# Kernel optimization log

Measured on AMD Instinct MI355X. Metric: run time of the kernel, lower is better.

The kernel has to match this reference:

```python
import jax, jax.numpy as jnp
import numpy as np
from jax import lax

B, N, C, HEADS = 4096, 49, 256, 8
HD = C // HEADS
SCALE = HD ** -0.5
BRANCHES = [(1, 0), (2, 0), (3, 1), (4, 2)]  # (dilation, padding) for d1..d4


def setup_inputs() -> dict:
    key = jax.random.key(0)
    ks = jax.random.split(key, 24)
    f = lambda i, shape: jax.random.normal(ks[i], shape, dtype=jnp.float32) * 0.05
    inp = {"x": jax.random.normal(ks[0], (B, N, C), dtype=jnp.float32)}
    inp["wq"] = f(1, (C, C)); inp["bq"] = f(2, (C,))
    for j in range(4):
        inp[f"wd{j+1}"] = f(3 + 4 * j, (C, 1, 3, 3))
        inp[f"bd{j+1}"] = f(4 + 4 * j, (C,))
        inp[f"wp{j+1}"] = f(5 + 4 * j, (2 * C, C))
        inp[f"bp{j+1}"] = f(6 + 4 * j, (2 * C,))
    inp["wproj"] = f(19, (C, C)); inp["bproj"] = f(20, (C,))
    return inp


def _branch(x4, wd, bd, wp, bp, dil, pad):
    # depthwise 3x3 stride-2 dilated conv
    d = lax.conv_general_dilated(
        x4, wd, window_strides=(2, 2), padding=[(pad, pad), (pad, pad)],
        rhs_dilation=(dil, dil), dimension_numbers=('NCHW', 'OIHW', 'NCHW'),
        feature_group_count=C) + bd[None, :, None, None]
    # pointwise 1x1 conv C -> 2C
    p = jnp.einsum('oc,bchw->bohw', wp, d) + bp[None, :, None, None]
    # replicate torch's reshape(B,C,-1).permute(0,2,1).reshape(B,-1,2,h,hd).permute(2,0,3,1,4)
    p = p.reshape(B, C, -1).transpose(0, 2, 1)
    p = p.reshape(B, -1, 2, HEADS, HD).transpose(2, 0, 3, 1, 4)
    return p[0], p[1]  # k, v: (B, HEADS, hw, HD)


def _forward(x, wq, bq, wd1, bd1, wp1, bp1, wd2, bd2, wp2, bp2,
             wd3, bd3, wp3, bp3, wd4, bd4, wp4, bp4, wproj, bproj):
    H = int(N ** 0.5)
    x4 = x.transpose(0, 2, 1).reshape(B, C, H, H)
    params = [(wd1, bd1, wp1, bp1), (wd2, bd2, wp2, bp2),
              (wd3, bd3, wp3, bp3), (wd4, bd4, wp4, bp4)]
    ks_, vs_ = [], []
    for (wd, bd, wp, bp), (dil, pad) in zip(params, BRANCHES):
        k_, v_ = _branch(x4, wd, bd, wp, bp, dil, pad)
        ks_.append(k_); vs_.append(v_)
    k = jnp.concatenate(ks_, axis=2)  # (B, HEADS, 21, HD)
    v = jnp.concatenate(vs_, axis=2)
    q = (jnp.einsum('bnc,oc->bno', x, wq) + bq)
    q = q.reshape(B, N, HEADS, HD).transpose(0, 2, 1, 3) * SCALE  # (B, H, N, HD)
    attn = jax.nn.softmax(jnp.einsum('bhnd,bhmd->bhnm', q, k), axis=-1)
    out = jnp.einsum('bhnm,bhmd->bhnd', attn, v)
    out = out.transpose(0, 2, 1, 3).reshape(B, N, C)
    return jnp.einsum('bnc,oc->bno', out, wproj) + bproj


def reference(x, wq, bq, wd1, bd1, wp1, bp1, wd2, bd2, wp2, bp2,
              wd3, bd3, wp3, bp3, wd4, bd4, wp4, bp4, wproj, bproj):
    return _forward(x, wq, bq, wd1, bd1, wp1, bp1, wd2, bd2, wp2, bp2,
                    wd3, bd3, wp3, bp3, wd4, bd4, wp4, bp4, wproj, bproj)
```

## Files before the change

### kernel.cpp

```cpp
#include <hip/hip_runtime.h>
#include <stdint.h>

typedef __attribute__((ext_vector_type(8))) short bf16x8;
typedef __attribute__((ext_vector_type(8))) unsigned short u16x8;
typedef __attribute__((ext_vector_type(4))) float f32x4;
typedef __attribute__((ext_vector_type(2))) uint32_t u32x2;

#define DEV __device__ __forceinline__

constexpr size_t WQ_PK    = 0;
constexpr size_t WPROJ_PK = 65536;
constexpr size_t WP_PK    = 131072;
constexpr size_t KVBUF    = 655360;

constexpr float SCALE_Q  = 0.17677669529663687f;

DEV uint16_t f2bf(float f){
  uint32_t u = __builtin_bit_cast(uint32_t, f);
  u += 0x7fffu + ((u >> 16) & 1u);
  return (uint16_t)(u >> 16);
}

DEV uint32_t cvtpk(float a, float b){
  uint32_t r;
  asm("v_cvt_pk_bf16_f32 %0, %1, %2" : "=v"(r) : "v"(a), "v"(b));
  return r;
}

DEV u16x8 extract_par(u16x8 a, u16x8 b, uint32_t sel){
  union U { u16x8 v; uint32_t d[4]; } A, B, R;
  A.v = a; B.v = b;
  R.d[0] = __builtin_amdgcn_perm(A.d[1], A.d[0], sel);
  R.d[1] = __builtin_amdgcn_perm(A.d[3], A.d[2], sel);
  R.d[2] = __builtin_amdgcn_perm(B.d[1], B.d[0], sel);
  R.d[3] = __builtin_amdgcn_perm(B.d[3], B.d[2], sel);
  return R.v;
}

__global__ __launch_bounds__(256) void k_prepack(
    const float* __restrict__ wq,  const float* __restrict__ wp1,
    const float* __restrict__ wp2, const float* __restrict__ wp3,
    const float* __restrict__ wp4, const float* __restrict__ wproj,
    uint16_t* __restrict__ ws)
{
  int f = blockIdx.x * 256 + threadIdx.x;
  const float* src; uint16_t* dst; int g;
  if (f < 8192)       { src = wq;    dst = ws + WQ_PK;    g = f; }
  else if (f < 16384) { src = wproj; dst = ws + WPROJ_PK; g = f - 8192; }
  else {
    int j = (f - 16384) >> 14;
    src = j == 0 ? wp1 : j == 1 ? wp2 : j == 2 ? wp3 : wp4;
    dst = ws + WP_PK + (size_t)j * 131072;
    g = (f - 16384) & 16383;
  }
  int l = g & 63, kt = (g >> 6) & 7, nt = g >> 9;
  int n  = nt * 16 + (l & 15);
  int k0 = kt * 32 + (l >> 4) * 8;
  const float* s = src + (size_t)n * 256 + k0;
  u16x8 v;
  #pragma unroll
  for (int j = 0; j < 8; ++j) v[j] = f2bf(s[j]);
  *reinterpret_cast<u16x8*>(dst + (size_t)g * 8) = v;
}

__global__ __launch_bounds__(512, 2) void k_kv(
    const float* __restrict__ x,
    const float* __restrict__ wd1, const float* __restrict__ bd1, const float* __restrict__ bp1,
    const float* __restrict__ wd2, const float* __restrict__ bd2, const float* __restrict__ bp2,
    const float* __restrict__ wd3, const float* __restrict__ bd3, const float* __restrict__ bp3,
    const float* __restrict__ wd4, const float* __restrict__ bd4, const float* __restrict__ bp4,
    const uint16_t* __restrict__ ws, uint16_t* __restrict__ kvbuf)
{
  extern __shared__ char smem[];
  const int t = threadIdx.x, lane = t & 63, w = t >> 6;
  const int q4 = lane >> 4, c15 = lane & 15;
  const int b0 = blockIdx.x * 8;

  constexpr int DILA[4] = {1,2,3,4}, PADA[4] = {0,0,1,2}, OWA[4] = {3,2,2,2};
  constexpr int HWA[4]  = {9,4,4,4}, OFFA[4] = {0,9,13,17}, MTA[4] = {5,2,2,2};

  {
    const int c = t & 255, half = t >> 8;
    for (int pass = 0; pass < 4; ++pass){
      const int bh = pass * 2 + half;
      float xr[49];
      #pragma unroll
      for (int p = 0; p < 49; ++p)
        xr[p] = x[((size_t)(b0 + bh) * 49 + p) * 256 + c];
      #pragma unroll
      for (int j = 0; j < 4; ++j){
        const float* wdp = j==0?wd1:j==1?wd2:j==2?wd3:wd4;
        const float* bdp = j==0?bd1:j==1?bd2:j==2?bd3:bd4;
        float wv[9];
        #pragma unroll
        for (int q = 0; q < 9; ++q) wv[q] = wdp[c * 9 + q];
        const float bdv = bdp[c];
        #pragma unroll
        for (int oy = 0; oy < OWA[j]; ++oy)
        #pragma unroll
        for (int ox = 0; ox < OWA[j]; ++ox){
          float acc = bdv;
          #pragma unroll
          for (int ky = 0; ky < 3; ++ky){
            const int yy = oy * 2 - PADA[j] + ky * DILA[j];
            if (yy < 0 || yy > 6) continue;
            #pragma unroll
            for (int kx = 0; kx < 3; ++kx){
              const int xx = ox * 2 - PADA[j] + kx * DILA[j];
              if (xx < 0 || xx > 6) continue;
              acc += xr[yy * 7 + xx] * wv[ky * 3 + kx];
            }
          }
          const int row = bh * 21 + OFFA[j] + oy * OWA[j] + ox;
          *reinterpret_cast<uint16_t*>(smem + ((row * 512 + c * 2) ^ ((row & 7) << 4))) = f2bf(acc);
        }
      }
    }
  }
  __syncthreads();

  #pragma unroll
  for (int j = 0; j < 4; ++j){
    const uint16_t* pk = ws + WP_PK + (size_t)j * 131072;
    const float* bpp = j==0?bp1:j==1?bp2:j==2?bp3:bp4;
    const int hw = HWA[j], off = OFFA[j], MV = hw * 8, ST = MTA[j];
    for (int st = 0; st < ST; ++st){
      const int sl = st * 16 + c15;
      const bool sv = sl < MV;
      const int svc = sv ? sl : 0;
      const int bh = svc / hw, sp = svc - bh * hw;
      const int arow = bh * 21 + off + sp;
      f32x4 acc[4] = {};
      #pragma unroll
      for (int kt = 0; kt < 8; ++kt){
        bf16x8 bfr = *reinterpret_cast<const bf16x8*>(smem + ((arow * 512 + kt * 64 + q4 * 16) ^ ((arow & 7) << 4)));
        #pragma unroll
        for (int ot = 0; ot < 4; ++ot){
          bf16x8 aw = *reinterpret_cast<const bf16x8*>(pk + (size_t)(((w * 4 + ot) * 8 + kt) * 64 + lane) * 8);
          acc[ot] = __builtin_amdgcn_mfma_f32_16x16x32_bf16(aw, bfr, acc[ot], 0, 0, 0);
        }
      }
      if (sv){
        const size_t grow = ((size_t)(b0 + bh) * 21 + off + sp) * 512;
        #pragma unroll
        for (int ot = 0; ot < 4; ++ot){
          const int ob = w * 64 + ot * 16 + q4 * 4;
          const f32x4 vb = *reinterpret_cast<const f32x4*>(bpp + ob);
          u32x2 pkv;
          pkv[0] = cvtpk(acc[ot][0] + vb[0], acc[ot][1] + vb[1]);
          pkv[1] = cvtpk(acc[ot][2] + vb[2], acc[ot][3] + vb[3]);
          *reinterpret_cast<u32x2*>(kvbuf + grow + ob) = pkv;
        }
      }
    }
  }
}

__global__ __launch_bounds__(512, 4) void k_attn(
    const float* __restrict__ x, const float* __restrict__ bq,
    const float* __restrict__ bproj, const uint16_t* __restrict__ ws,
    float* __restrict__ out)
{
  extern __shared__ char smem[];
  constexpr int OSB = 32768;
  const int t = threadIdx.x, lane = t & 63, w = t >> 6;
  const int q4 = lane >> 4, c15 = lane & 15;
  const size_t b = blockIdx.x;
  const uint16_t* wq_pk    = ws + WQ_PK;
  const uint16_t* wproj_pk = ws + WPROJ_PK;
  const uint16_t* kvbuf    = ws + KVBUF;

  const int sh4 = t >> 7, m = (t >> 2) & 31, dch = (t & 3) * 8;
  const bool mv = m < 21;
  uint32_t selK = 0x05040100u, selV = 0x05040100u;
  const uint16_t *rk = kvbuf, *rv = kvbuf;
  if (mv){
    int off, hw;
    if (m < 9)       { off = 0;  hw = 9; }
    else if (m < 13) { off = 9;  hw = 4; }
    else if (m < 17) { off = 13; hw = 4; }
    else             { off = 17; hw = 4; }
    const int ml = m - off;
    const int c2k = 2 * ml,     ek = c2k >= hw ? 1 : 0, sk = c2k - ek * hw;
    const int c2v = 2 * ml + 1, ev = c2v >= hw ? 1 : 0, sv = c2v - ev * hw;
    selK = ek ? 0x07060302u : 0x05040100u;
    selV = ev ? 0x07060302u : 0x05040100u;
    const int o0 = 2 * (sh4 * 32 + dch);
    rk = kvbuf + (b * 21 + off + sk) * 512 + o0;
    rv = kvbuf + (b * 21 + off + sv) * 512 + o0;
  }
  u16x8 L0 = {}, L1 = {}, L2 = {}, L3 = {};
  if (mv){
    L0 = *reinterpret_cast<const u16x8*>(rk);
    L1 = *reinterpret_cast<const u16x8*>(rk + 8);
    L2 = *reinterpret_cast<const u16x8*>(rv);
    L3 = *reinterpret_cast<const u16x8*>(rv + 8);
  }

  {
    const int r = t >> 3, c0 = (t & 7) * 32;
    u16x8 vv[4] = {};
    if (r < 49){
      const float* src = x + (b * 49 + r) * 256 + c0;
      #pragma unroll
      for (int jj = 0; jj < 4; ++jj){
        f32x4 f0 = *reinterpret_cast<const f32x4*>(src + jj * 8);
        f32x4 f1 = *reinterpret_cast<const f32x4*>(src + jj * 8 + 4);
        union { u16x8 v; uint32_t d[4]; } R;
        R.d[0] = cvtpk(f0[0], f0[1]);
        R.d[1] = cvtpk(f0[2], f0[3]);
        R.d[2] = cvtpk(f1[0], f1[1]);
        R.d[3] = cvtpk(f1[2], f1[3]);
        vv[jj] = R.v;
      }
    }
    #pragma unroll
    for (int jj = 0; jj < 4; ++jj)
      *reinterpret_cast<u16x8*>(smem + ((r * 512 + c0 * 2 + jj * 16) ^ ((r & 7) << 4))) = vv[jj];
  }
  __syncthreads();

  f32x4 qacc[2][4] = {};
  #pragma unroll 2
  for (int kt = 0; kt < 8; ++kt){
    bf16x8 bx[4];
    #pragma unroll
    for (int nt = 0; nt < 4; ++nt){
      const int row = nt * 16 + c15;
      bx[nt] = *reinterpret_cast<const bf16x8*>(smem + ((row * 512 + kt * 64 + q4 * 16) ^ ((row & 7) << 4)));
    }
    #pragma unroll
    for (int mt = 0; mt < 2; ++mt){
      bf16x8 aw = *reinterpret_cast<const bf16x8*>(wq_pk + (size_t)(((w * 2 + mt) * 8 + kt) * 64 + lane) * 8);
      #pragma unroll
      for (int nt = 0; nt < 4; ++nt)
        qacc[mt][nt] = __builtin_amdgcn_mfma_f32_16x16x32_bf16(aw, bx[nt], qacc[mt][nt], 0, 0, 0);
    }
  }
  #pragma unroll
  for (int mt = 0; mt < 2; ++mt){
    const int ob = w * 32 + mt * 16 + q4 * 4;
    const f32x4 vb = *reinterpret_cast<const f32x4*>(bq + ob);
    #pragma unroll
    for (int nt = 0; nt < 4; ++nt){
      const int row = nt * 16 + c15;
      u32x2 pkq;
      pkq[0] = cvtpk((qacc[mt][nt][0] + vb[0]) * SCALE_Q, (qacc[mt][nt][1] + vb[1]) * SCALE_Q);
      pkq[1] = cvtpk((qacc[mt][nt][2] + vb[2]) * SCALE_Q, (qacc[mt][nt][3] + vb[3]) * SCALE_Q);
      *reinterpret_cast<u32x2*>(smem + OSB + ((row * 512 + ob * 2) ^ ((row & 7) << 4))) = pkq;
    }
  }
  __syncthreads();

  for (int p = 0; p < 2; ++p){
    {
      u16x8 kf = extract_par(L0, L1, selK);
      u16x8 vf = extract_par(L2, L3, selV);
      *reinterpret_cast<u16x8*>(smem + sh4 * 2048 + ((m * 64 + dch * 2) ^ ((m & 7) << 4))) = kf;
      #pragma unroll
      for (int jj = 0; jj < 8; ++jj){
        const int d = dch + jj;
        *reinterpret_cast<uint16_t*>(smem + 8192 + sh4 * 2048 + ((d * 64 + m * 2) ^ ((d & 7) << 4))) = vf[jj];
      }
      if (p == 0 && mv){
        L0 = *reinterpret_cast<const u16x8*>(rk + 256);
        L1 = *reinterpret_cast<const u16x8*>(rk + 264);
        L2 = *reinterpret_cast<const u16x8*>(rv + 256);
        L3 = *reinterpret_cast<const u16x8*>(rv + 264);
      }
    }
    __syncthreads();

    const int h4 = w >> 1, wh = w & 1;
    const int hcol = (p * 4 + h4) * 64;
    const int pabase = 16384 + h4 * 4096;

    bf16x8 bk[2];
    #pragma unroll
    for (int nt = 0; nt < 2; ++nt){
      const int m0 = nt * 16 + c15;
      bk[nt] = *reinterpret_cast<const bf16x8*>(smem + h4 * 2048 + ((m0 * 64 + q4 * 16) ^ ((m0 & 7) << 4)));
    }
    f32x4 sacc[2][2];
    #pragma unroll
    for (int mt = 0; mt < 2; ++mt){
      const int row = wh * 32 + mt * 16 + c15;
      bf16x8 aq = *reinterpret_cast<const bf16x8*>(smem + OSB + ((row * 512 + hcol + q4 * 16) ^ ((row & 7) << 4)));
      #pragma unroll
      for (int nt = 0; nt < 2; ++nt){
        f32x4 z = {};
        sacc[mt][nt] = __builtin_amdgcn_mfma_f32_16x16x32_bf16(aq, bk[nt], z, 0, 0, 0);
      }
    }
    const bool ok1 = c15 < 5;
    #pragma unroll
    for (int mt = 0; mt < 2; ++mt)
      #pragma unroll
      for (int i = 0; i < 4; ++i){
        const float s0 = sacc[mt][0][i];
        const float s1 = sacc[mt][1][i];
        float mx = fmaxf(s0, ok1 ? s1 : -3.0e38f);
        #pragma unroll
        for (int dd = 1; dd < 16; dd <<= 1) mx = fmaxf(mx, __shfl_xor(mx, dd));
        const float e0 = __expf(s0 - mx);
        const float e1 = ok1 ? __expf(s1 - mx) : 0.f;
        float sm = e0 + e1;
        #pragma unroll
        for (int dd = 1; dd < 16; dd <<= 1) sm += __shfl_xor(sm, dd);
        const float inv = 1.0f / sm;
        const int pr = wh * 32 + mt * 16 + q4 * 4 + i;
        *reinterpret_cast<uint16_t*>(smem + pabase + ((pr * 64 + c15 * 2) ^ ((pr & 7) << 4))) = f2bf(e0 * inv);
        *reinterpret_cast<uint16_t*>(smem + pabase + ((pr * 64 + (c15 + 16) * 2) ^ ((pr & 7) << 4))) = f2bf(e1 * inv);
      }
    f32x4 oacc[2][2];
    #pragma unroll
    for (int mt = 0; mt < 2; ++mt){
      const int pr = wh * 32 + mt * 16 + c15;
      bf16x8 ap = *reinterpret_cast<const bf16x8*>(smem + pabase + ((pr * 64 + q4 * 16) ^ ((pr & 7) << 4)));
      #pragma unroll
      for (int nt = 0; nt < 2; ++nt){
        const int d0 = nt * 16 + c15;
        bf16x8 bv = *reinterpret_cast<const bf16x8*>(smem + 8192 + h4 * 2048 + ((d0 * 64 + q4 * 16) ^ ((d0 & 7) << 4)));
        f32x4 z = {};
        oacc[mt][nt] = __builtin_amdgcn_mfma_f32_16x16x32_bf16(ap, bv, z, 0, 0, 0);
      }
    }
    #pragma unroll
    for (int mt = 0; mt < 2; ++mt)
      #pragma unroll
      for (int nt = 0; nt < 2; ++nt)
        #pragma unroll
        for (int i = 0; i < 4; ++i){
          const int row = wh * 32 + mt * 16 + q4 * 4 + i;
          const int colb = hcol + (nt * 16 + c15) * 2;
          *reinterpret_cast<uint16_t*>(smem + OSB + ((row * 512 + colb) ^ ((row & 7) << 4))) = f2bf(oacc[mt][nt][i]);
        }
    __syncthreads();
  }

  f32x4 pacc[2][4] = {};
  #pragma unroll 2
  for (int kt = 0; kt < 8; ++kt){
    bf16x8 bo[4];
    #pragma unroll
    for (int nt = 0; nt < 4; ++nt){
      const int row = nt * 16 + c15;
      bo[nt] = *reinterpret_cast<const bf16x8*>(smem + OSB + ((row * 512 + kt * 64 + q4 * 16) ^ ((row & 7) << 4)));
    }
    #pragma unroll
    for (int mt = 0; mt < 2; ++mt){
      bf16x8 aw = *reinterpret_cast<const bf16x8*>(wproj_pk + (size_t)(((w * 2 + mt) * 8 + kt) * 64 + lane) * 8);
      #pragma unroll
      for (int nt = 0; nt < 4; ++nt)
        pacc[mt][nt] = __builtin_amdgcn_mfma_f32_16x16x32_bf16(aw, bo[nt], pacc[mt][nt], 0, 0, 0);
    }
  }
  #pragma unroll
  for (int mt = 0; mt < 2; ++mt){
    const int ob = w * 32 + mt * 16 + q4 * 4;
    const f32x4 vb = *reinterpret_cast<const f32x4*>(bproj + ob);
    #pragma unroll
    for (int nt = 0; nt < 4; ++nt){
      const int n = nt * 16 + c15;
      if (n < 49)
        *reinterpret_cast<f32x4*>(out + (b * 49 + n) * 256 + ob) = pacc[mt][nt] + vb;
    }
  }
}

extern "C" void kernel_launch(void* const* d_in, const int* in_sizes, int n_in,
                              void* d_out, int out_size, void* d_ws, size_t ws_size,
                              hipStream_t stream)
{
  const float* x     = (const float*)d_in[0];
  const float* wq    = (const float*)d_in[1];
  const float* bq    = (const float*)d_in[2];
  const float* wd1   = (const float*)d_in[3];
  const float* bd1   = (const float*)d_in[4];
  const float* wp1   = (const float*)d_in[5];
  const float* bp1   = (const float*)d_in[6];
  const float* wd2   = (const float*)d_in[7];
  const float* bd2   = (const float*)d_in[8];
  const float* wp2   = (const float*)d_in[9];
  const float* bp2   = (const float*)d_in[10];
  const float* wd3   = (const float*)d_in[11];
  const float* bd3   = (const float*)d_in[12];
  const float* wp3   = (const float*)d_in[13];
  const float* bp3   = (const float*)d_in[14];
  const float* wd4   = (const float*)d_in[15];
  const float* bd4   = (const float*)d_in[16];
  const float* wp4   = (const float*)d_in[17];
  const float* bp4   = (const float*)d_in[18];
  const float* wproj = (const float*)d_in[19];
  const float* bproj = (const float*)d_in[20];
  uint16_t* ws = (uint16_t*)d_ws;
  float* out = (float*)d_out;

  k_prepack<<<320, 256, 0, stream>>>(wq, wp1, wp2, wp3, wp4, wproj, ws);
  k_kv<<<512, 512, 86016, stream>>>(x, wd1, bd1, bp1, wd2, bd2, bp2,
                                    wd3, bd3, bp3, wd4, bd4, bp4,
                                    ws, ws + KVBUF);
  k_attn<<<4096, 512, 65536, stream>>>(x, bq, bproj, ws, out);
}
```

Baseline: 329.8 us.

## Shrink attention LDS footprint and process two heads per pass to raise occupancy

The attention kernel now reuses the x staging buffer for Q/output, with an extra barrier before the Q writes, which cuts dynamic LDS from 64KB to 48KB. The launch-bounds occupancy hint goes from 4 to 6 blocks. Heads are now processed two per pass over four passes instead of four per pass over two, and each thread loads only a K or a V fragment, which halves the prefetch registers. The aim is more resident blocks per CU, at the cost of extra barriers and passes that add serialization.

```diff
diff --git a/kernel.cpp b/kernel.cpp
--- a/kernel.cpp
+++ b/kernel.cpp
@@ -156,13 +156,12 @@
   }
 }
 
-__global__ __launch_bounds__(512, 4) void k_attn(
+__global__ __launch_bounds__(512, 6) void k_attn(
     const float* __restrict__ x, const float* __restrict__ bq,
     const float* __restrict__ bproj, const uint16_t* __restrict__ ws,
     float* __restrict__ out)
 {
   extern __shared__ char smem[];
-  constexpr int OSB = 32768;
   const int t = threadIdx.x, lane = t & 63, w = t >> 6;
   const int q4 = lane >> 4, c15 = lane & 15;
   const size_t b = blockIdx.x;
@@ -170,10 +169,11 @@
   const uint16_t* wproj_pk = ws + WPROJ_PK;
   const uint16_t* kvbuf    = ws + KVBUF;
 
-  const int sh4 = t >> 7, m = (t >> 2) & 31, dch = (t & 3) * 8;
+  const int dch = (t & 3) * 8, m = (t >> 2) & 31, unit = t >> 7;
+  const int hh_s = unit >> 1, kind = unit & 1;
   const bool mv = m < 21;
-  uint32_t selK = 0x05040100u, selV = 0x05040100u;
-  const uint16_t *rk = kvbuf, *rv = kvbuf;
+  uint32_t sel = 0x05040100u;
+  const uint16_t* rg = kvbuf;
   if (mv){
     int off, hw;
     if (m < 9)       { off = 0;  hw = 9; }
@@ -181,20 +181,15 @@
     else if (m < 17) { off = 13; hw = 4; }
     else             { off = 17; hw = 4; }
     const int ml = m - off;
-    const int c2k = 2 * ml,     ek = c2k >= hw ? 1 : 0, sk = c2k - ek * hw;
-    const int c2v = 2 * ml + 1, ev = c2v >= hw ? 1 : 0, sv = c2v - ev * hw;
-    selK = ek ? 0x07060302u : 0x05040100u;
-    selV = ev ? 0x07060302u : 0x05040100u;
-    const int o0 = 2 * (sh4 * 32 + dch);
-    rk = kvbuf + (b * 21 + off + sk) * 512 + o0;
-    rv = kvbuf + (b * 21 + off + sv) * 512 + o0;
-  }
-  u16x8 L0 = {}, L1 = {}, L2 = {}, L3 = {};
+    const int c2 = 2 * ml + kind;
+    const int e = c2 >= hw ? 1 : 0, s = c2 - e * hw;
+    sel = e ? 0x07060302u : 0x05040100u;
+    rg = kvbuf + (b * 21 + off + s) * 512 + 2 * (hh_s * 32 + dch);
+  }
+  u16x8 L0 = {}, L1 = {};
   if (mv){
-    L0 = *reinterpret_cast<const u16x8*>(rk);
-    L1 = *reinterpret_cast<const u16x8*>(rk + 8);
-    L2 = *reinterpret_cast<const u16x8*>(rv);
-    L3 = *reinterpret_cast<const u16x8*>(rv + 8);
+    L0 = *reinterpret_cast<const u16x8*>(rg);
+    L1 = *reinterpret_cast<const u16x8*>(rg + 8);
   }
 
   {
@@ -237,6 +232,8 @@
         qacc[mt][nt] = __builtin_amdgcn_mfma_f32_16x16x32_bf16(aw, bx[nt], qacc[mt][nt], 0, 0, 0);
     }
   }
+  __syncthreads();
+
   #pragma unroll
   for (int mt = 0; mt < 2; ++mt){
     const int ob = w * 32 + mt * 16 + q4 * 4;
@@ -247,94 +244,83 @@
       u32x2 pkq;
       pkq[0] = cvtpk((qacc[mt][nt][0] + vb[0]) * SCALE_Q, (qacc[mt][nt][1] + vb[1]) * SCALE_Q);
       pkq[1] = cvtpk((qacc[mt][nt][2] + vb[2]) * SCALE_Q, (qacc[mt][nt][3] + vb[3]) * SCALE_Q);
-      *reinterpret_cast<u32x2*>(smem + OSB + ((row * 512 + ob * 2) ^ ((row & 7) << 4))) = pkq;
+      *reinterpret_cast<u32x2*>(smem + ((row * 512 + ob * 2) ^ ((row & 7) << 4))) = pkq;
     }
   }
   __syncthreads();
 
-  for (int p = 0; p < 2; ++p){
+  const int hh = w >> 2, wh2 = w & 3;
+  for (int p = 0; p < 4; ++p){
     {
-      u16x8 kf = extract_par(L0, L1, selK);
-      u16x8 vf = extract_par(L2, L3, selV);
-      *reinterpret_cast<u16x8*>(smem + sh4 * 2048 + ((m * 64 + dch * 2) ^ ((m & 7) << 4))) = kf;
-      #pragma unroll
-      for (int jj = 0; jj < 8; ++jj){
-        const int d = dch + jj;
-        *reinterpret_cast<uint16_t*>(smem + 8192 + sh4 * 2048 + ((d * 64 + m * 2) ^ ((d & 7) << 4))) = vf[jj];
-      }
-      if (p == 0 && mv){
-        L0 = *reinterpret_cast<const u16x8*>(rk + 256);
-        L1 = *reinterpret_cast<const u16x8*>(rk + 264);
-        L2 = *reinterpret_cast<const u16x8*>(rv + 256);
-        L3 = *reinterpret_cast<const u16x8*>(rv + 264);
+      u16x8 vfr = {};
+      if (mv) vfr = extract_par(L0, L1, sel);
+      if (kind == 0){
+        *reinterpret_cast<u16x8*>(smem + 32768 + hh_s * 2048 + ((m * 64 + dch * 2) ^ ((m & 7) << 4))) = vfr;
+      } else {
+        #pragma unroll
+        for (int jj = 0; jj < 8; ++jj){
+          const int d = dch + jj;
+          *reinterpret_cast<uint16_t*>(smem + 36864 + hh_s * 2048 + ((d * 64 + m * 2) ^ ((d & 7) << 4))) = vfr[jj];
+        }
+      }
+      if (p < 3 && mv){
+        L0 = *reinterpret_cast<const u16x8*>(rg + (p + 1) * 128);
+        L1 = *reinterpret_cast<const u16x8*>(rg + (p + 1) * 128 + 8);
       }
     }
     __syncthreads();
 
-    const int h4 = w >> 1, wh = w & 1;
-    const int hcol = (p * 4 + h4) * 64;
-    const int pabase = 16384 + h4 * 4096;
-
-    bf16x8 bk[2];
+    const int hcolb = (p * 2 + hh) * 64;
+    const int kbK = 32768 + hh * 2048;
+    const int kbV = 36864 + hh * 2048;
+    const int pb  = 40960 + hh * 4096;
+
+    const int arowq = wh2 * 16 + c15;
+    bf16x8 aq = *reinterpret_cast<const bf16x8*>(smem + ((arowq * 512 + hcolb + q4 * 16) ^ ((arowq & 7) << 4)));
+    f32x4 sacc[2];
     #pragma unroll
     for (int nt = 0; nt < 2; ++nt){
       const int m0 = nt * 16 + c15;
-      bk[nt] = *reinterpret_cast<const bf16x8*>(smem + h4 * 2048 + ((m0 * 64 + q4 * 16) ^ ((m0 & 7) << 4)));
-    }
-    f32x4 sacc[2][2];
-    #pragma unroll
-    for (int mt = 0; mt < 2; ++mt){
-      const int row = wh * 32 + mt * 16 + c15;
-      bf16x8 aq = *reinterpret_cast<const bf16x8*>(smem + OSB + ((row * 512 + hcol + q4 * 16) ^ ((row & 7) << 4)));
-      #pragma unroll
-      for (int nt = 0; nt < 2; ++nt){
-        f32x4 z = {};
-        sacc[mt][nt] = __builtin_amdgcn_mfma_f32_16x16x32_bf16(aq, bk[nt], z, 0, 0, 0);
-      }
+      bf16x8 bk = *reinterpret_cast<const bf16x8*>(smem + kbK + ((m0 * 64 + q4 * 16) ^ ((m0 & 7) << 4)));
+      f32x4 z = {};
+      sacc[nt] = __builtin_amdgcn_mfma_f32_16x16x32_bf16(aq, bk, z, 0, 0, 0);
     }
     const bool ok1 = c15 < 5;
     #pragma unroll
-    for (int mt = 0; mt < 2; ++mt)
+    for (int i = 0; i < 4; ++i){
+      const float s0 = sacc[0][i];
+      const float s1 = sacc[1][i];
+      float mx = fmaxf(s0, ok1 ? s1 : -3.0e38f);
+      #pragma unroll
+      for (int dd = 1; dd < 16; dd <<= 1) mx = fmaxf(mx, __shfl_xor(mx, dd));
+      const float e0 = __expf(s0 - mx);
+      const float e1 = ok1 ? __expf(s1 - mx) : 0.f;
+      float sm = e0 + e1;
+      #pragma unroll
+      for (int dd = 1; dd < 16; dd <<= 1) sm += __shfl_xor(sm, dd);
+      const float inv = 1.0f / sm;
+      const int pr = wh2 * 16 + q4 * 4 + i;
+      *reinterpret_cast<uint16_t*>(smem + pb + ((pr * 64 + c15 * 2) ^ ((pr & 7) << 4))) = f2bf(e0 * inv);
+      *reinterpret_cast<uint16_t*>(smem + pb + ((pr * 64 + (c15 + 16) * 2) ^ ((pr & 7) << 4))) = f2bf(e1 * inv);
+    }
+    const int prow = wh2 * 16 + c15;
+    bf16x8 ap = *reinterpret_cast<const bf16x8*>(smem + pb + ((prow * 64 + q4 * 16) ^ ((prow & 7) << 4)));
+    f32x4 oacc[2];
+    #pragma unroll
+    for (int nt = 0; nt < 2; ++nt){
+      const int d0 = nt * 16 + c15;
+      bf16x8 bv = *reinterpret_cast<const bf16x8*>(smem + kbV + ((d0 * 64 + q4 * 16) ^ ((d0 & 7) << 4)));
+      f32x4 z = {};
+      oacc[nt] = __builtin_amdgcn_mfma_f32_16x16x32_bf16(ap, bv, z, 0, 0, 0);
+    }
+    #pragma unroll
+    for (int nt = 0; nt < 2; ++nt)
       #pragma unroll
       for (int i = 0; i < 4; ++i){
-        const float s0 = sacc[mt][0][i];
-        const float s1 = sacc[mt][1][i];
-        float mx = fmaxf(s0, ok1 ? s1 : -3.0e38f);
-        #pragma unroll
-        for (int dd = 1; dd < 16; dd <<= 1) mx = fmaxf(mx, __shfl_xor(mx, dd));
-        const float e0 = __expf(s0 - mx);
-        const float e1 = ok1 ? __expf(s1 - mx) : 0.f;
-        float sm = e0 + e1;
-        #pragma unroll
-        for (int dd = 1; dd < 16; dd <<= 1) sm += __shfl_xor(sm, dd);
-        const float inv = 1.0f / sm;
-        const int pr = wh * 32 + mt * 16 + q4 * 4 + i;
-        *reinterpret_cast<uint16_t*>(smem + pabase + ((pr * 64 + c15 * 2) ^ ((pr & 7) << 4))) = f2bf(e0 * inv);
-        *reinterpret_cast<uint16_t*>(smem + pabase + ((pr * 64 + (c15 + 16) * 2) ^ ((pr & 7) << 4))) = f2bf(e1 * inv);
-      }
-    f32x4 oacc[2][2];
-    #pragma unroll
-    for (int mt = 0; mt < 2; ++mt){
-      const int pr = wh * 32 + mt * 16 + c15;
-      bf16x8 ap = *reinterpret_cast<const bf16x8*>(smem + pabase + ((pr * 64 + q4 * 16) ^ ((pr & 7) << 4)));
-      #pragma unroll
-      for (int nt = 0; nt < 2; ++nt){
-        const int d0 = nt * 16 + c15;
-        bf16x8 bv = *reinterpret_cast<const bf16x8*>(smem + 8192 + h4 * 2048 + ((d0 * 64 + q4 * 16) ^ ((d0 & 7) << 4)));
-        f32x4 z = {};
-        oacc[mt][nt] = __builtin_amdgcn_mfma_f32_16x16x32_bf16(ap, bv, z, 0, 0, 0);
-      }
-    }
-    #pragma unroll
-    for (int mt = 0; mt < 2; ++mt)
-      #pragma unroll
-      for (int nt = 0; nt < 2; ++nt)
-        #pragma unroll
-        for (int i = 0; i < 4; ++i){
-          const int row = wh * 32 + mt * 16 + q4 * 4 + i;
-          const int colb = hcol + (nt * 16 + c15) * 2;
-          *reinterpret_cast<uint16_t*>(smem + OSB + ((row * 512 + colb) ^ ((row & 7) << 4))) = f2bf(oacc[mt][nt][i]);
-        }
+        const int row = wh2 * 16 + q4 * 4 + i;
+        const int colb = hcolb + (nt * 16 + c15) * 2;
+        *reinterpret_cast<uint16_t*>(smem + ((row * 512 + colb) ^ ((row & 7) << 4))) = f2bf(oacc[nt][i]);
+      }
     __syncthreads();
   }
 
@@ -345,7 +331,7 @@
     #pragma unroll
     for (int nt = 0; nt < 4; ++nt){
       const int row = nt * 16 + c15;
-      bo[nt] = *reinterpret_cast<const bf16x8*>(smem + OSB + ((row * 512 + kt * 64 + q4 * 16) ^ ((row & 7) << 4)));
+      bo[nt] = *reinterpret_cast<const bf16x8*>(smem + ((row * 512 + kt * 64 + q4 * 16) ^ ((row & 7) << 4)));
     }
     #pragma unroll
     for (int mt = 0; mt < 2; ++mt){
@@ -400,5 +386,5 @@
   k_kv<<<512, 512, 86016, stream>>>(x, wd1, bd1, bp1, wd2, bd2, bp2,
                                     wd3, bd3, bp3, wd4, bd4, bp4,
                                     ws, ws + KVBUF);
-  k_attn<<<4096, 512, 65536, stream>>>(x, bq, bproj, ws, out);
-}
+  k_attn<<<4096, 512, 49152, stream>>>(x, bq, bproj, ws, out);
+}
```

Result: faster. 320.1 us (-2.9%).
